# Optimization experiments

Hardware: AMD Instinct MI355X
Metric: run time of the kernel (lower is better)

## Reference

```python
import jax, jax.numpy as jnp
import numpy as np

EPS = 1e-4

def mp_weight(w):
    # MP_GeoLinear eval-mode weight: normalize then scale by gain/sqrt(fan_in)
    w32 = w.astype(jnp.float32)
    norm = jnp.linalg.norm(w32, axis=1, keepdims=True)          # [out,1]
    fan_in = w.shape[1]
    denom = EPS + norm / np.sqrt(fan_in)                        # torch.add(eps, norm, alpha=sqrt(1/fan_in))
    wn = w32 / denom
    return (wn / np.sqrt(fan_in)).astype(w.dtype)               # gain=1


def setup_inputs() -> dict:
    key = jax.random.key(0)
    k1, k2, k3, k4 = jax.random.split(key, 4)
    N, E, C = 100000, 1600000, 128
    x = jax.random.normal(k1, (N, C), dtype=jnp.float32)
    edge_index = jax.random.randint(k2, (2, E), 0, N, dtype=jnp.int64)
    w_neigh = jax.random.normal(k3, (C, C), dtype=jnp.float32)
    w_res = jax.random.normal(k4, (C, C), dtype=jnp.float32)
    return {"x": x, "edge_index": edge_index, "w_neigh": w_neigh, "w_res": w_res}


def reference(x, edge_index, w_neigh, w_res):
    N = x.shape[0]
    row, col = edge_index[0], edge_index[1]            # source, target
    # degree of target nodes
    deg = jax.ops.segment_sum(jnp.ones_like(col, dtype=x.dtype), col, num_segments=N)
    deg_inv = jnp.where(deg > 0, deg ** -0.5, 0.0)     # inf -> 0
    norm = deg_inv[col]                                 # [E]
    # message: x_j * norm, aggregate: scatter-add into col
    msg = x[row] * norm[:, None]                        # [E,C]
    agg = jax.ops.segment_sum(msg, col, num_segments=N) # [N,C]
    neighbourhood = agg @ mp_weight(w_neigh).T
    residual = x @ mp_weight(w_res).T
    # mp_sum(residual, neighbourhood, t=0.5) = (a+b)/sqrt(2)
    join = (residual + neighbourhood) / np.sqrt(2.0)
    out = jnp.where((deg > 0)[:, None], join, residual)
    return out
```

## Files before the change

kernel.cpp:

```cpp
#include <hip/hip_runtime.h>
#include <hip/hip_bf16.h>

#define C 128
#define INV_SQRT2 0.7071067811865476f
#define NB 1024
#define BS 128
#define EPB 4096
#define CAPB 2560
#define AGS 68

typedef __attribute__((ext_vector_type(8))) short short8;
typedef __attribute__((ext_vector_type(4))) float f32x4;

__device__ inline ushort f2b(float f) {
    __hip_bfloat16 h = __float2bfloat16(f);
    return __builtin_bit_cast(ushort, h);
}


__global__ __launch_bounds__(512) void k_front(
    const int* __restrict__ row, const int* __restrict__ col, int E, int nblk,
    int* __restrict__ gcursor, unsigned int* __restrict__ recs,
    const float4* __restrict__ x, ushort* __restrict__ xb, int n4, int castBlocks,
    const float* __restrict__ w_res, const float* __restrict__ w_neigh,
    ushort* __restrict__ Bp)
{
    __shared__ int hist[NB];
    __shared__ int lbase[NB];
    int b = blockIdx.x;
    int t = threadIdx.x;
    if (b < nblk) {
        hist[t] = 0; hist[t + 512] = 0;
        __syncthreads();
        int base = b * EPB;
        #pragma unroll
        for (int i = 0; i < EPB / 512; i++) {
            int e = base + i * 512 + t;
            if (e < E) atomicAdd(&hist[col[e] >> 7], 1);
        }
        __syncthreads();
        #pragma unroll
        for (int kx = 0; kx < 2; kx++) {
            int bb = t + kx * 512;
            int h = hist[bb];
            lbase[bb] = h ? atomicAdd(&gcursor[bb], h) : 0;
        }
        __syncthreads();
        hist[t] = 0; hist[t + 512] = 0;
        __syncthreads();
        #pragma unroll
        for (int i = 0; i < EPB / 512; i++) {
            int e = base + i * 512 + t;
            if (e < E) {
                int c = col[e];
                int kk = c >> 7;
                int p = atomicAdd(&hist[kk], 1) + lbase[kk];
                if (p < CAPB)
                    recs[(size_t)kk * CAPB + p] =
                        ((unsigned int)(c & 127) << 24) | (unsigned int)row[e];
            }
        }
    } else if (b < nblk + castBlocks) {
        int i = (b - nblk) * 512 + t;
        if (i < n4) {
            float4 v = x[i];
            ushort4 o;
            o.x = f2b(v.x); o.y = f2b(v.y); o.z = f2b(v.z); o.w = f2b(v.w);
            *(ushort4*)(xb + (size_t)i * 4) = o;
        }
    } else {
        int r = (b - nblk - castBlocks) * 8 + (t >> 6);
        int h = r >> 7;
        int i = r & 127;
        const float* w = h ? w_neigh : w_res;
        int lane = t & 63;
        float a = w[i * C + lane];
        float bb = w[i * C + lane + 64];
        float ss = a * a + bb * bb;
        #pragma unroll
        for (int off = 32; off > 0; off >>= 1) ss += __shfl_down(ss, off);
        ss = __shfl(ss, 0);
        float norm = sqrtf(ss);
        float denom = 1e-4f + norm * 0.08838834764831845f;
        float scale = 1.0f / (denom * 11.313708498984761f);
        int c1 = lane, c2 = lane + 64;
        Bp[(size_t)(h * 16 + (c1 >> 3)) * 1024 + i * 8 + (c1 & 7)] = f2b(a * scale);
        Bp[(size_t)(h * 16 + (c2 >> 3)) * 1024 + i * 8 + (c2 & 7)] = f2b(bb * scale);
    }
}


#define ACCUM(v) do { \
    acc[0] += __builtin_bit_cast(float, (v).x << 16); \
    acc[1] += __builtin_bit_cast(float, (v).x & 0xffff0000u); \
    acc[2] += __builtin_bit_cast(float, (v).y << 16); \
    acc[3] += __builtin_bit_cast(float, (v).y & 0xffff0000u); \
    acc[4] += __builtin_bit_cast(float, (v).z << 16); \
    acc[5] += __builtin_bit_cast(float, (v).z & 0xffff0000u); \
    acc[6] += __builtin_bit_cast(float, (v).w << 16); \
    acc[7] += __builtin_bit_cast(float, (v).w & 0xffff0000u); \
} while (0)

__global__ __launch_bounds__(512, 4) void k_fused(
    const unsigned int* __restrict__ recs, const int* __restrict__ gcursor,
    const ushort* __restrict__ xb, const ushort* __restrict__ Bp,
    float* __restrict__ out, int N)
{
    __shared__ int lidx[CAPB];
    __shared__ int shist[BS];
    __shared__ int sexcl[BS];
    __shared__ int scur[BS];
    __shared__ uint sAgg[BS * AGS];

    int k = blockIdx.x;
    int t = threadIdx.x;
    int cnt = gcursor[k];
    if (cnt > CAPB) cnt = CAPB;
    const unsigned int* rb = recs + (size_t)k * CAPB;

    if (t < BS) shist[t] = 0;
    __syncthreads();
    for (int i = t; i < cnt; i += 512)
        atomicAdd(&shist[rb[i] >> 24], 1);
    __syncthreads();
    if (t < 64) {
        int a = shist[t], b = shist[t + 64];
        int ia = a, ib = b;
        #pragma unroll
        for (int off = 1; off < 64; off <<= 1) {
            int ya = __shfl_up(ia, off);
            int yb = __shfl_up(ib, off);
            if (t >= off) { ia += ya; ib += yb; }
        }
        int tot0 = __shfl(ia, 63);
        int e0 = ia - a;
        int e1 = ib - b + tot0;
        sexcl[t] = e0;      scur[t] = e0;
        sexcl[t + 64] = e1; scur[t + 64] = e1;
    }
    __syncthreads();
    for (int i = t; i < cnt; i += 512) {
        unsigned int r = rb[i];
        int c = r >> 24;
        int p = atomicAdd(&scur[c], 1);
        lidx[p] = (int)(r & 0xFFFFFF);
    }
    __syncthreads();

    int lane = t & 63;
    int wave = t >> 6;
    int s  = lane >> 4;
    int cl = lane & 15;
    #pragma unroll 1
    for (int ln = wave * 16; ln < wave * 16 + 16; ln++) {
        int s0 = sexcl[ln];
        int d  = shist[ln];
        float acc[8];
        #pragma unroll
        for (int i = 0; i < 8; i++) acc[i] = 0.f;
        for (int j = 0; j < d; j += 8) {
            int j0 = j + s, j1 = j + 4 + s;
            int i0 = lidx[s0 + (j0 < d ? j0 : d - 1)];
            int i1 = lidx[s0 + (j1 < d ? j1 : d - 1)];
            uint4 va = *(const uint4*)(xb + ((size_t)i0 << 7) + (cl << 3));
            uint4 vb = *(const uint4*)(xb + ((size_t)i1 << 7) + (cl << 3));
            if (j0 >= d) va = make_uint4(0, 0, 0, 0);
            if (j1 >= d) vb = make_uint4(0, 0, 0, 0);
            ACCUM(va);
            ACCUM(vb);
        }
        #pragma unroll
        for (int i = 0; i < 8; i++) {
            acc[i] += __shfl_xor(acc[i], 16);
            acc[i] += __shfl_xor(acc[i], 32);
        }
        float dd = (d > 0) ? rsqrtf((float)d) : 0.f;
        if (lane < 16) {
            uint4 o;
            o.x = (uint)f2b(acc[0] * dd) | ((uint)f2b(acc[1] * dd) << 16);
            o.y = (uint)f2b(acc[2] * dd) | ((uint)f2b(acc[3] * dd) << 16);
            o.z = (uint)f2b(acc[4] * dd) | ((uint)f2b(acc[5] * dd) << 16);
            o.w = (uint)f2b(acc[6] * dd) | ((uint)f2b(acc[7] * dd) << 16);
            *(uint4*)&sAgg[ln * AGS + cl * 4] = o;
        }
    }
    __syncthreads();

    int quad = lane >> 4;
    int l16  = lane & 15;
    long gbase = (long)k * BS;
    int arow = wave * 16 + l16;
    long garow = gbase + arow;
    if (garow >= N) garow = N - 1;

    f32x4 oacc[8];
    #pragma unroll
    for (int nt = 0; nt < 8; nt++) oacc[nt] = (f32x4){0.f, 0.f, 0.f, 0.f};

    #pragma unroll
    for (int kk = 0; kk < 8; kk++) {
        short8 af;
        if (kk < 4) {
            af = *(const short8*)(xb + garow * C + kk * 32 + quad * 8);
        } else {
            af = *(const short8*)&sAgg[arow * AGS + (kk - 4) * 16 + quad * 4];
        }
        #pragma unroll
        for (int nt = 0; nt < 8; nt++) {
            short8 bf = *(const short8*)(Bp +
                ((size_t)((kk * 4 + quad) * 128) + nt * 16 + l16) * 8);
            oacc[nt] = __builtin_amdgcn_mfma_f32_16x16x32_bf16(af, bf, oacc[nt], 0, 0, 0);
        }
    }

    #pragma unroll
    for (int r2 = 0; r2 < 4; r2++) {
        int rl = wave * 16 + quad * 4 + r2;
        long rowg = gbase + rl;
        if (rowg < N) {
            float sc = (shist[rl] > 0) ? INV_SQRT2 : 1.0f;
            float* o = out + rowg * C + l16;
            #pragma unroll
            for (int nt = 0; nt < 8; nt++)
                __builtin_nontemporal_store(oacc[nt][r2] * sc, &o[nt * 16]);
        }
    }
}


extern "C" void kernel_launch(void* const* d_in, const int* in_sizes, int n_in,
                              void* d_out, int out_size, void* d_ws, size_t ws_size,
                              hipStream_t stream) {
    const float* x       = (const float*)d_in[0];
    const int*   eidx    = (const int*)d_in[1];
    const float* w_neigh = (const float*)d_in[2];
    const float* w_res   = (const float*)d_in[3];
    float* out = (float*)d_out;

    int N = in_sizes[0] / C;
    int E = in_sizes[1] / 2;
    const int* row = eidx;
    const int* col = eidx + E;

    char* ws = (char*)d_ws;
    size_t off = 0;
    auto alloc = [&](size_t bytes) {
        size_t o = off;
        off += (bytes + 511) & ~(size_t)511;
        return o;
    };
    int nblk = (E + EPB - 1) / EPB;

    int*    gcursor    = (int*)(ws + alloc(NB * 4));
    unsigned int* recs = (unsigned int*)(ws + alloc((size_t)NB * CAPB * 4));
    ushort* Bp         = (ushort*)(ws + alloc((size_t)32 * 1024 * 2));
    ushort* xb         = (ushort*)(ws + alloc((size_t)N * C * 2 + 65536));
    (void)ws_size;

    hipMemsetAsync(gcursor, 0, NB * 4, stream);

    int nbuckets = (N + BS - 1) / BS;
    int n4 = N * C / 4;
    int castBlocks = (n4 + 511) / 512;

    k_front<<<nblk + castBlocks + 32, 512, 0, stream>>>(
        row, col, E, nblk, gcursor, recs,
        (const float4*)x, xb, n4, castBlocks, w_res, w_neigh, Bp);
    k_fused<<<nbuckets, 512, 0, stream>>>(recs, gcursor, xb, Bp, out, N);
}
```

Measured before the change: 219.5 us.

## Move per-bucket neighbour index list to global memory with padded segments and zero row

Stores the sorted neighbour index list in a global scratch buffer instead of LDS, padding each node's segment to a multiple of eight with a sentinel index that points at an added zero row of the bf16 feature copy. This removes the bounds checks and masking in the gather loop. The loop is unrolled to four gathers per iteration, and the launch bound is raised to allow more resident blocks. The final barrier before the matmul is replaced by an LDS waitcnt. The index lookups now go through global or cache memory instead of LDS, and dropping the barrier is only safe if each wave reads back only the aggregated rows it wrote itself.

After: 221.4 us. Within noise of the previous version (+0.9%).

```diff
diff --git a/kernel.cpp b/kernel.cpp
--- a/kernel.cpp
+++ b/kernel.cpp
@@ -7,6 +7,7 @@
 #define BS 128
 #define EPB 4096
 #define CAPB 2560
+#define LIDX_CAP 3456
 #define AGS 68
 
 typedef __attribute__((ext_vector_type(8))) short short8;
@@ -68,6 +69,10 @@
             o.x = f2b(v.x); o.y = f2b(v.y); o.z = f2b(v.z); o.w = f2b(v.w);
             *(ushort4*)(xb + (size_t)i * 4) = o;
         }
+        if (b == nblk && t < 32) {
+            ushort4 z = make_ushort4(0, 0, 0, 0);
+            *(ushort4*)(xb + ((size_t)n4 << 2) + (t << 2)) = z;
+        }
     } else {
         int r = (b - nblk - castBlocks) * 8 + (t >> 6);
         int h = r >> 7;
@@ -101,12 +106,11 @@
     acc[7] += __builtin_bit_cast(float, (v).w & 0xffff0000u); \
 } while (0)
 
-__global__ __launch_bounds__(512, 4) void k_fused(
+__global__ __launch_bounds__(512, 8) void k_fused(
     const unsigned int* __restrict__ recs, const int* __restrict__ gcursor,
     const ushort* __restrict__ xb, const ushort* __restrict__ Bp,
-    float* __restrict__ out, int N)
+    int* __restrict__ lidxg, float* __restrict__ out, int N)
 {
-    __shared__ int lidx[CAPB];
     __shared__ int shist[BS];
     __shared__ int sexcl[BS];
     __shared__ int scur[BS];
@@ -117,6 +121,7 @@
     int cnt = gcursor[k];
     if (cnt > CAPB) cnt = CAPB;
     const unsigned int* rb = recs + (size_t)k * CAPB;
+    int* lw = lidxg + (size_t)k * LIDX_CAP;
 
     if (t < BS) shist[t] = 0;
     __syncthreads();
@@ -125,7 +130,8 @@
     __syncthreads();
     if (t < 64) {
         int a = shist[t], b = shist[t + 64];
-        int ia = a, ib = b;
+        int pa = (a + 7) & ~7, pb = (b + 7) & ~7;
+        int ia = pa, ib = pb;
         #pragma unroll
         for (int off = 1; off < 64; off <<= 1) {
             int ya = __shfl_up(ia, off);
@@ -133,8 +139,8 @@
             if (t >= off) { ia += ya; ib += yb; }
         }
         int tot0 = __shfl(ia, 63);
-        int e0 = ia - a;
-        int e1 = ib - b + tot0;
+        int e0 = ia - pa;
+        int e1 = ib - pb + tot0;
         sexcl[t] = e0;      scur[t] = e0;
         sexcl[t + 64] = e1; scur[t + 64] = e1;
     }
@@ -143,7 +149,12 @@
         unsigned int r = rb[i];
         int c = r >> 24;
         int p = atomicAdd(&scur[c], 1);
-        lidx[p] = (int)(r & 0xFFFFFF);
+        lw[p] = (int)(r & 0xFFFFFF);
+    }
+    if (t < BS) {
+        int d = shist[t], b0 = sexcl[t];
+        int pe = b0 + ((d + 7) & ~7);
+        for (int p = b0 + d; p < pe; p++) lw[p] = N;
     }
     __syncthreads();
 
@@ -151,21 +162,34 @@
     int wave = t >> 6;
     int s  = lane >> 4;
     int cl = lane & 15;
+    const ushort* xcl = xb + (cl << 3);
     #pragma unroll 1
     for (int ln = wave * 16; ln < wave * 16 + 16; ln++) {
-        int s0 = sexcl[ln];
+        int j  = sexcl[ln];
         int d  = shist[ln];
+        int jend = j + ((d + 7) & ~7);
         float acc[8];
         #pragma unroll
         for (int i = 0; i < 8; i++) acc[i] = 0.f;
-        for (int j = 0; j < d; j += 8) {
-            int j0 = j + s, j1 = j + 4 + s;
-            int i0 = lidx[s0 + (j0 < d ? j0 : d - 1)];
-            int i1 = lidx[s0 + (j1 < d ? j1 : d - 1)];
-            uint4 va = *(const uint4*)(xb + ((size_t)i0 << 7) + (cl << 3));
-            uint4 vb = *(const uint4*)(xb + ((size_t)i1 << 7) + (cl << 3));
-            if (j0 >= d) va = make_uint4(0, 0, 0, 0);
-            if (j1 >= d) vb = make_uint4(0, 0, 0, 0);
+        for (; j + 16 <= jend; j += 16) {
+            int i0 = lw[j + s];
+            int i1 = lw[j + 4 + s];
+            int i2 = lw[j + 8 + s];
+            int i3 = lw[j + 12 + s];
+            uint4 va = *(const uint4*)(xcl + ((size_t)i0 << 7));
+            uint4 vb = *(const uint4*)(xcl + ((size_t)i1 << 7));
+            uint4 vc = *(const uint4*)(xcl + ((size_t)i2 << 7));
+            uint4 vd = *(const uint4*)(xcl + ((size_t)i3 << 7));
+            ACCUM(va);
+            ACCUM(vb);
+            ACCUM(vc);
+            ACCUM(vd);
+        }
+        if (j < jend) {
+            int i0 = lw[j + s];
+            int i1 = lw[j + 4 + s];
+            uint4 va = *(const uint4*)(xcl + ((size_t)i0 << 7));
+            uint4 vb = *(const uint4*)(xcl + ((size_t)i1 << 7));
             ACCUM(va);
             ACCUM(vb);
         }
@@ -184,7 +208,7 @@
             *(uint4*)&sAgg[ln * AGS + cl * 4] = o;
         }
     }
-    __syncthreads();
+    asm volatile("s_waitcnt lgkmcnt(0)" ::: "memory");
 
     int quad = lane >> 4;
     int l16  = lane & 15;
@@ -255,6 +279,7 @@
     unsigned int* recs = (unsigned int*)(ws + alloc((size_t)NB * CAPB * 4));
     ushort* Bp         = (ushort*)(ws + alloc((size_t)32 * 1024 * 2));
     ushort* xb         = (ushort*)(ws + alloc((size_t)N * C * 2 + 65536));
+    int*    lidxg      = (int*)(ws + alloc((size_t)NB * LIDX_CAP * 4));
     (void)ws_size;
 
     hipMemsetAsync(gcursor, 0, NB * 4, stream);
@@ -266,5 +291,5 @@
     k_front<<<nblk + castBlocks + 32, 512, 0, stream>>>(
         row, col, E, nblk, gcursor, recs,
         (const float4*)x, xb, n4, castBlocks, w_res, w_neigh, Bp);
-    k_fused<<<nbuckets, 512, 0, stream>>>(recs, gcursor, xb, Bp, out, N);
-}
+    k_fused<<<nbuckets, 512, 0, stream>>>(recs, gcursor, xb, Bp, lidxg, out, N);
+}
```
